# Performance work log

Measured on AMD Instinct MI355X. Metric: run time of the kernel, lower is better.

Reference implementation:

```python
import jax, jax.numpy as jnp
import numpy as np
import math

FREQS = jnp.array([1., 2., 4., 8., 7., 5.], dtype=jnp.float32)  # default frequencies


def setup_inputs() -> dict:
    key = jax.random.key(0)
    k1, k2, k3 = jax.random.split(key, 3)
    B, N, H, F = 8, 4096, 256, 6
    x = jax.random.normal(k1, (B, N, H), dtype=jnp.float32)
    t = jax.random.uniform(k2, (B, 1), dtype=jnp.float32) * (2.0 * math.pi)
    oscillators = jax.random.normal(k3, (F, H, H), dtype=jnp.float32) * 0.1
    # phase_shifts[i] = i / F * pi, broadcast over hidden dim (matches torch init)
    phase_shifts = jnp.broadcast_to(
        (jnp.arange(F, dtype=jnp.float32) / F * math.pi)[:, None], (F, H)
    ).copy()
    return {"x": x, "t": t, "oscillators": oscillators, "phase_shifts": phase_shifts}


def reference(x, t, oscillators, phase_shifts):
    # resonator[b, f, h] = sin(freq_f * t[b, 0] + phase[f, h])
    res = jnp.sin(FREQS[None, :, None] * t[:, :, None] + phase_shifts[None, :, :])  # [B, F, H]
    # result[b, n, k] = sum_f (x[b, n, :] @ W_f)[k] * res[b, f, k]
    return jnp.einsum('bnh,fhk,bfk->bnk', x, oscillators, res)
```

## Files before the change

kernel.cpp:

```cpp
#include <hip/hip_runtime.h>
#include <hip/hip_bf16.h>


#define B_  8
#define N_  4096
#define H_  256

typedef __attribute__((ext_vector_type(8))) short s8v;
typedef __attribute__((ext_vector_type(4))) float f4v;

__global__ __launch_bounds__(256) void build_w(
    const float* __restrict__ osc,
    const float* __restrict__ t,
    const float* __restrict__ phase,
    __hip_bfloat16* __restrict__ Wt)
{
    const float freqs[6] = {1.f, 2.f, 4.f, 8.f, 7.f, 5.f};
    int idx = blockIdx.x * 256 + threadIdx.x;
    int b   = idx >> 16;
    int rem = idx & 65535;
    int n   = rem >> 8;
    int h   = rem & 255;
    float tb  = t[b];
    float acc = 0.f;
#pragma unroll
    for (int f = 0; f < 6; ++f) {
        float s = __sinf(freqs[f] * tb + phase[f * 256 + n]);
        acc += osc[f * 65536 + h * 256 + n] * s;
    }
    Wt[idx] = __float2bfloat16(acc);
}

#define LDSTRIDE 40

__global__ __launch_bounds__(512) void gemm(
    const float* __restrict__ X,
    const __hip_bfloat16* __restrict__ Wt,
    float* __restrict__ out)
{
    __shared__ short As[128 * LDSTRIDE];
    __shared__ short Bs[128 * LDSTRIDE];

    const int b     = blockIdx.z;
    const int mTile = blockIdx.x;
    const int nTile = blockIdx.y;

    const int tid    = threadIdx.x;
    const int lane   = tid & 63;
    const int wave   = tid >> 6;
    const int lane15 = lane & 15;
    const int quad   = lane >> 4;
    const int wm     = wave >> 1;
    const int wn     = wave & 1;

    const float* Xb          = X   + (size_t)b * N_ * H_ + (size_t)mTile * 128 * H_;
    const __hip_bfloat16* Wb = Wt  + (size_t)b * H_ * H_ + (size_t)nTile * 128 * H_;
    float* Ob                = out + (size_t)b * N_ * H_ + (size_t)mTile * 128 * H_ + nTile * 128;

    const int srow = tid >> 2;
    const int skq  = tid & 3;

    const float* pa          = Xb + (size_t)srow * H_ + skq * 8;
    const __hip_bfloat16* pb = Wb + (size_t)srow * H_ + skq * 8;

    f4v acc[2][4] = {};

    float4 a0 = *(const float4*)(pa);
    float4 a1 = *(const float4*)(pa + 4);
    uint4  bv = *(const uint4*)(pb);

    for (int it = 0; it < 8; ++it) {
        union { __hip_bfloat162 h[4]; uint4 q; } cv;
        cv.h[0] = __float22bfloat162_rn(make_float2(a0.x, a0.y));
        cv.h[1] = __float22bfloat162_rn(make_float2(a0.z, a0.w));
        cv.h[2] = __float22bfloat162_rn(make_float2(a1.x, a1.y));
        cv.h[3] = __float22bfloat162_rn(make_float2(a1.z, a1.w));
        *(uint4*)(&As[srow * LDSTRIDE + skq * 8]) = cv.q;
        *(uint4*)(&Bs[srow * LDSTRIDE + skq * 8]) = bv;
        __syncthreads();

        if (it < 7) {
            const float4* na          = (const float4*)(pa + (it + 1) * 32);
            a0 = na[0];
            a1 = na[1];
            bv = *(const uint4*)(pb + (it + 1) * 32);
        }

        s8v af[2], bf[4];
#pragma unroll
        for (int mt = 0; mt < 2; ++mt)
            af[mt] = *(const s8v*)(&As[(wm * 32 + mt * 16 + lane15) * LDSTRIDE + quad * 8]);
#pragma unroll
        for (int nt = 0; nt < 4; ++nt)
            bf[nt] = *(const s8v*)(&Bs[(wn * 64 + nt * 16 + lane15) * LDSTRIDE + quad * 8]);

#pragma unroll
        for (int mt = 0; mt < 2; ++mt)
#pragma unroll
            for (int nt = 0; nt < 4; ++nt)
                acc[mt][nt] = __builtin_amdgcn_mfma_f32_16x16x32_bf16(
                    af[mt], bf[nt], acc[mt][nt], 0, 0, 0);
        __syncthreads();
    }

#pragma unroll
    for (int mt = 0; mt < 2; ++mt) {
#pragma unroll
        for (int r = 0; r < 4; ++r) {
            int row = wm * 32 + mt * 16 + quad * 4 + r;
            float* po = Ob + (size_t)row * H_ + wn * 64 + lane15;
#pragma unroll
            for (int nt = 0; nt < 4; ++nt)
                po[nt * 16] = acc[mt][nt][r];
        }
    }
}

extern "C" void kernel_launch(void* const* d_in, const int* in_sizes, int n_in,
                              void* d_out, int out_size, void* d_ws, size_t ws_size,
                              hipStream_t stream) {
    const float* x     = (const float*)d_in[0];
    const float* t     = (const float*)d_in[1];
    const float* osc   = (const float*)d_in[2];
    const float* phase = (const float*)d_in[3];
    __hip_bfloat16* Wt = (__hip_bfloat16*)d_ws;
    float* out = (float*)d_out;

    build_w<<<2048, 256, 0, stream>>>(osc, t, phase, Wt);

    dim3 grid(32, 2, 8);
    gemm<<<grid, 512, 0, stream>>>(x, Wt, out);
}
```

Baseline: 109.7 us.

## Coalesce W build via LDS transpose and retile GEMM to full-N 64-row blocks

```diff
diff --git a/kernel.cpp b/kernel.cpp
--- a/kernel.cpp
+++ b/kernel.cpp
@@ -16,83 +16,113 @@
     __hip_bfloat16* __restrict__ Wt)
 {
     const float freqs[6] = {1.f, 2.f, 4.f, 8.f, 7.f, 5.f};
-    int idx = blockIdx.x * 256 + threadIdx.x;
-    int b   = idx >> 16;
-    int rem = idx & 65535;
-    int n   = rem >> 8;
-    int h   = rem & 255;
-    float tb  = t[b];
-    float acc = 0.f;
+    __shared__ float tr[16 * 68];
+
+    const int b  = blockIdx.z;
+    const int n0 = blockIdx.y * 64;
+    const int h0 = blockIdx.x * 128;
+    const int tid = threadIdx.x;
+
+    const float tb = t[b];
+    const int nr = (tid & 15) * 4;
+    const int hr = tid >> 4;
+    float s[6][4];
 #pragma unroll
-    for (int f = 0; f < 6; ++f) {
-        float s = __sinf(freqs[f] * tb + phase[f * 256 + n]);
-        acc += osc[f * 65536 + h * 256 + n] * s;
+    for (int f = 0; f < 6; ++f)
+#pragma unroll
+        for (int j = 0; j < 4; ++j)
+            s[f][j] = __sinf(freqs[f] * tb + phase[f * 256 + n0 + nr + j]);
+
+    const int nw = tid >> 2;
+    const int hw = (tid & 3) * 4;
+    __hip_bfloat16* wout = Wt + (size_t)b * 65536 + (size_t)(n0 + nw) * 256 + h0;
+
+    for (int hp = 0; hp < 8; ++hp) {
+        const int h = h0 + hp * 16 + hr;
+        float4 acc = make_float4(0.f, 0.f, 0.f, 0.f);
+#pragma unroll
+        for (int f = 0; f < 6; ++f) {
+            float4 o = *(const float4*)&osc[f * 65536 + h * 256 + n0 + nr];
+            acc.x += o.x * s[f][0];
+            acc.y += o.y * s[f][1];
+            acc.z += o.z * s[f][2];
+            acc.w += o.w * s[f][3];
+        }
+        __syncthreads();
+        *(float4*)&tr[hr * 68 + nr] = acc;
+        __syncthreads();
+        float v0 = tr[(hw + 0) * 68 + nw];
+        float v1 = tr[(hw + 1) * 68 + nw];
+        float v2 = tr[(hw + 2) * 68 + nw];
+        float v3 = tr[(hw + 3) * 68 + nw];
+        union { __hip_bfloat162 h2[2]; unsigned long long q; } cv;
+        cv.h2[0] = __float22bfloat162_rn(make_float2(v0, v1));
+        cv.h2[1] = __float22bfloat162_rn(make_float2(v2, v3));
+        *(unsigned long long*)(wout + hp * 16 + hw) = cv.q;
     }
-    Wt[idx] = __float2bfloat16(acc);
 }
 
-#define LDSTRIDE 40
+#define LDST 40
 
-__global__ __launch_bounds__(512) void gemm(
+__global__ __launch_bounds__(512, 4) void gemm(
     const float* __restrict__ X,
     const __hip_bfloat16* __restrict__ Wt,
     float* __restrict__ out)
 {
-    __shared__ short As[128 * LDSTRIDE];
-    __shared__ short Bs[128 * LDSTRIDE];
+    __shared__ short As[64 * LDST];
+    __shared__ short Bs[256 * LDST];
 
-    const int b     = blockIdx.z;
+    const int b     = blockIdx.y;
     const int mTile = blockIdx.x;
-    const int nTile = blockIdx.y;
 
     const int tid    = threadIdx.x;
     const int lane   = tid & 63;
     const int wave   = tid >> 6;
     const int lane15 = lane & 15;
     const int quad   = lane >> 4;
-    const int wm     = wave >> 1;
-    const int wn     = wave & 1;
+    const int wm     = wave >> 2;
+    const int wn     = wave & 3;
 
-    const float* Xb          = X   + (size_t)b * N_ * H_ + (size_t)mTile * 128 * H_;
-    const __hip_bfloat16* Wb = Wt  + (size_t)b * H_ * H_ + (size_t)nTile * 128 * H_;
-    float* Ob                = out + (size_t)b * N_ * H_ + (size_t)mTile * 128 * H_ + nTile * 128;
+    const float* Xb          = X   + (size_t)b * N_ * H_ + (size_t)mTile * 64 * H_;
+    const __hip_bfloat16* Wb = Wt  + (size_t)b * H_ * H_;
+    float* Ob                = out + (size_t)b * N_ * H_ + (size_t)mTile * 64 * H_;
 
-    const int srow = tid >> 2;
-    const int skq  = tid & 3;
+    const int arow = tid >> 3;
+    const int aseg = tid & 7;
+    const float* pa = Xb + (size_t)arow * H_ + aseg * 4;
 
-    const float* pa          = Xb + (size_t)srow * H_ + skq * 8;
-    const __hip_bfloat16* pb = Wb + (size_t)srow * H_ + skq * 8;
+    const int brow = tid >> 1;
+    const int bh   = tid & 1;
+    const __hip_bfloat16* pb = Wb + (size_t)brow * H_ + bh * 16;
 
     f4v acc[2][4] = {};
 
-    float4 a0 = *(const float4*)(pa);
-    float4 a1 = *(const float4*)(pa + 4);
-    uint4  bv = *(const uint4*)(pb);
+    float4 av = *(const float4*)pa;
+    uint4  bv0 = *(const uint4*)(pb);
+    uint4  bv1 = *(const uint4*)(pb + 8);
 
     for (int it = 0; it < 8; ++it) {
-        union { __hip_bfloat162 h[4]; uint4 q; } cv;
-        cv.h[0] = __float22bfloat162_rn(make_float2(a0.x, a0.y));
-        cv.h[1] = __float22bfloat162_rn(make_float2(a0.z, a0.w));
-        cv.h[2] = __float22bfloat162_rn(make_float2(a1.x, a1.y));
-        cv.h[3] = __float22bfloat162_rn(make_float2(a1.z, a1.w));
-        *(uint4*)(&As[srow * LDSTRIDE + skq * 8]) = cv.q;
-        *(uint4*)(&Bs[srow * LDSTRIDE + skq * 8]) = bv;
+        union { __hip_bfloat162 h2[2]; unsigned long long q; } cv;
+        cv.h2[0] = __float22bfloat162_rn(make_float2(av.x, av.y));
+        cv.h2[1] = __float22bfloat162_rn(make_float2(av.z, av.w));
+        *(unsigned long long*)(&As[arow * LDST + aseg * 4]) = cv.q;
+        *(uint4*)(&Bs[brow * LDST + bh * 16 + 0]) = bv0;
+        *(uint4*)(&Bs[brow * LDST + bh * 16 + 8]) = bv1;
         __syncthreads();
 
         if (it < 7) {
-            const float4* na          = (const float4*)(pa + (it + 1) * 32);
-            a0 = na[0];
-            a1 = na[1];
-            bv = *(const uint4*)(pb + (it + 1) * 32);
+            av  = *(const float4*)(pa + (it + 1) * 32);
+            bv0 = *(const uint4*)(pb + (it + 1) * 32);
+            bv1 = *(const uint4*)(pb + (it + 1) * 32 + 8);
         }
 
         s8v af[2], bf[4];
 #pragma unroll
         for (int mt = 0; mt < 2; ++mt)
-            af[mt] = *(const s8v*)(&As[(wm * 32 + mt * 16 + lane15) * LDSTRIDE + quad * 8]);
+            af[mt] = *(const s8v*)(&As[(wm * 32 + mt * 16 + lane15) * LDST + quad * 8]);
 #pragma unroll
         for (int nt = 0; nt < 4; ++nt)
-            bf[nt] = *(const s8v*)(&Bs[(wn * 64 + nt * 16 + lane15) * LDSTRIDE + quad * 8]);
+            bf[nt] = *(const s8v*)(&Bs[(wn * 64 + nt * 16 + lane15) * LDST + quad * 8]);
 
 #pragma unroll
         for (int mt = 0; mt < 2; ++mt)
@@ -126,8 +156,9 @@
     __hip_bfloat16* Wt = (__hip_bfloat16*)d_ws;
     float* out = (float*)d_out;
 
-    build_w<<<2048, 256, 0, stream>>>(osc, t, phase, Wt);
+    dim3 gw(2, 4, 8);
+    build_w<<<gw, 256, 0, stream>>>(osc, t, phase, Wt);
 
-    dim3 grid(32, 2, 8);
-    gemm<<<grid, 512, 0, stream>>>(x, Wt, out);
+    dim3 gg(64, 8);
+    gemm<<<gg, 512, 0, stream>>>(x, Wt, out);
 }
```

New measurement: 101.3 us. 1.08x faster.
